# Performance work log

Hardware: AMD Instinct MI355X
Metric: run time of the kernel (lower is better)

## Reference

```python
import jax, jax.numpy as jnp
import numpy as np

DM, DI, DS, DC, DTR, L = 512, 1024, 16, 4, 32, 2
Bb, N = 4, 1024


def layer_norm(x, w, b):
    mu = x.mean(-1, keepdims=True)
    v = ((x - mu) ** 2).mean(-1, keepdims=True)
    return (x - mu) * jax.lax.rsqrt(v + 1e-5) * w + b


def silu(x):
    return x * jax.nn.sigmoid(x)


def selective_ssm(u, p):
    in_w, cw, cb, xpw, dtw, dtb, alog, dd, ow = p
    xz = u @ in_w                        # [B,N,2*DI]
    xh, z = jnp.split(xz, 2, axis=-1)
    # causal depthwise conv over time
    xt = jnp.pad(xh.transpose(0, 2, 1), ((0, 0), (0, 0), (DC - 1, 0)))
    xc = jax.lax.conv_general_dilated(xt, cw[:, None, :], (1,), 'VALID', feature_group_count=DI)
    xh = silu(xc.transpose(0, 2, 1) + cb)
    dbl = xh @ xpw                       # [B,N,DTR+2*DS]
    dt = jax.nn.softplus(dbl[..., :DTR] @ dtw + dtb)   # [B,N,DI]
    Bm = dbl[..., DTR:DTR + DS]
    Cm = dbl[..., DTR + DS:]
    A = -jnp.exp(alog)                   # [DI,DS]

    def step(h, inp):
        dt_t, B_t, C_t, x_t = inp        # [B,DI],[B,DS],[B,DS],[B,DI]
        h = jnp.exp(dt_t[..., None] * A) * h + (dt_t * x_t)[..., None] * B_t[:, None, :]
        return h, jnp.einsum('bds,bs->bd', h, C_t)

    xs = (dt.transpose(1, 0, 2), Bm.transpose(1, 0, 2), Cm.transpose(1, 0, 2), xh.transpose(1, 0, 2))
    h0 = jnp.zeros((u.shape[0], DI, DS), u.dtype)
    _, ys = jax.lax.scan(step, h0, xs)
    y = ys.transpose(1, 0, 2) + dd * xh
    return (y * silu(z)) @ ow


def mamba_layer(h, p):
    n1w, n1b, in_w, cw, cb, xpw, dtw, dtb, alog, dd, ow, n2w, n2b, w1, b1, w2, b2 = p
    h = h + selective_ssm(layer_norm(h, n1w, n1b), (in_w, cw, cb, xpw, dtw, dtb, alog, dd, ow))
    hn = layer_norm(h, n2w, n2b)
    return h + (jax.nn.gelu(hn @ w1 + b1, approximate=False) @ w2 + b2), None


def run_stack(x, stack):
    h, _ = jax.lax.scan(mamba_layer, x, stack)
    return h


def setup_inputs() -> dict:
    key = jax.random.key(0)
    ks = iter(jax.random.split(key, 80))

    def w(shape, s=0.02):
        return jax.random.normal(next(ks), shape, jnp.float32) * s

    d = {"x": jax.random.normal(next(ks), (Bb, N, DM), jnp.float32)}
    for pre in ("f", "b"):
        d[pre + "_n1w"] = jnp.ones((L, DM)); d[pre + "_n1b"] = jnp.zeros((L, DM))
        d[pre + "_inw"] = w((L, DM, 2 * DI)); d[pre + "_cw"] = w((L, DI, DC), 0.1)
        d[pre + "_cb"] = jnp.zeros((L, DI)); d[pre + "_xpw"] = w((L, DI, DTR + 2 * DS))
        d[pre + "_dtw"] = w((L, DTR, DI), 0.1); d[pre + "_dtb"] = w((L, DI), 0.5)
        d[pre + "_alog"] = jnp.tile(jnp.log(jnp.arange(1, DS + 1, dtype=jnp.float32)), (L, DI, 1))
        d[pre + "_dd"] = jnp.ones((L, DI))
        d[pre + "_ow"] = w((L, DI, DM))
        d[pre + "_n2w"] = jnp.ones((L, DM)); d[pre + "_n2b"] = jnp.zeros((L, DM))
        d[pre + "_w1"] = w((L, DM, 4 * DM)); d[pre + "_b1"] = jnp.zeros((L, 4 * DM))
        d[pre + "_w2"] = w((L, 4 * DM, DM)); d[pre + "_b2"] = jnp.zeros((L, DM))
    d["aw1"] = w((DM, DM // 2)); d["ab1"] = jnp.zeros((DM // 2,))
    d["aw2"] = w((DM // 2, 1)); d["ab2"] = jnp.zeros((1,))
    d["nw"] = jnp.ones((2 * DM,)); d["nb"] = jnp.zeros((2 * DM,))
    return d


def reference(x, f_n1w, f_n1b, f_inw, f_cw, f_cb, f_xpw, f_dtw, f_dtb, f_alog, f_dd, f_ow, f_n2w, f_n2b, f_w1, f_b1, f_w2, f_b2, b_n1w, b_n1b, b_inw, b_cw, b_cb, b_xpw, b_dtw, b_dtb, b_alog, b_dd, b_ow, b_n2w, b_n2b, b_w1, b_b1, b_w2, b_b2, aw1, ab1, aw2, ab2, nw, nb):
    fstack = (f_n1w, f_n1b, f_inw, f_cw, f_cb, f_xpw, f_dtw, f_dtb, f_alog, f_dd, f_ow, f_n2w, f_n2b, f_w1, f_b1, f_w2, f_b2)
    bstack = (b_n1w, b_n1b, b_inw, b_cw, b_cb, b_xpw, b_dtw, b_dtb, b_alog, b_dd, b_ow, b_n2w, b_n2b, b_w1, b_b1, b_w2, b_b2)
    hf = run_stack(x, fstack)
    hb = jnp.flip(run_stack(jnp.flip(x, 1), bstack), 1)

    def attn(h):
        return jax.nn.softmax((jnp.tanh(h @ aw1 + ab1) @ aw2 + ab2)[..., 0], axis=-1)

    af = attn(hf)
    abw = attn(hb)
    zf = jnp.einsum('bn,bnd->bd', af, hf)
    zb = jnp.einsum('bn,bnd->bd', abw, hb)
    z = layer_norm(jnp.concatenate([zf, zb], axis=-1), nw, nb)
    return z, (af + abw) * 0.5
```

## Files before the change

### kernel.cpp

```cpp
#include <hip/hip_runtime.h>
#include <math.h>

constexpr int kDM   = 512;
constexpr int kDI   = 1024;
constexpr int kDS   = 16;
constexpr int kDC   = 4;
constexpr int kDTR  = 32;
constexpr int kL    = 2;
constexpr int kB    = 4;
constexpr int kN    = 1024;
constexpr int kB2   = 8;
constexpr int kROWS = kB2 * kN;
constexpr int kMDIR = kB * kN;

enum { EPI_NONE=0, EPI_SOFTPLUS=1, EPI_RESID=2, EPI_GELU=3, EPI_RESID_BIAS=4, EPI_TANH=5 };
enum { MODE_N=0, MODE_OTR=1, MODE_DBL=2, MODE_GATE=3 };

typedef __attribute__((ext_vector_type(8))) short bf16x8;
typedef __attribute__((ext_vector_type(4))) short bf16x4;
typedef __attribute__((ext_vector_type(4))) float f32x4;

__device__ __forceinline__ unsigned short f2bf(float f) {
    unsigned int u = __float_as_uint(f);
    return (unsigned short)((u + 0x7FFFu + ((u >> 16) & 1u)) >> 16);
}
__device__ __forceinline__ float b2f(unsigned short u) {
    return __uint_as_float((unsigned int)u << 16);
}
__device__ __forceinline__ bf16x4 pack4(const float* v) {
    union { unsigned short u[4]; bf16x4 t; } p;
#pragma unroll
    for (int j = 0; j < 4; j++) p.u[j] = f2bf(v[j]);
    return p.t;
}

struct WJobs { const float* s[13]; };
constexpr size_t O_INW_F = 0;
constexpr size_t O_INW_B = O_INW_F + 2u*512*2048;
constexpr size_t O_XPW_F = O_INW_B + 2u*512*2048;
constexpr size_t O_XPW_B = O_XPW_F + 2u*1024*64;
constexpr size_t O_DTW_F = O_XPW_B + 2u*1024*64;
constexpr size_t O_DTW_B = O_DTW_F + 2u*32*1024;
constexpr size_t O_OW_F  = O_DTW_B + 2u*32*1024;
constexpr size_t O_OW_B  = O_OW_F  + 2u*1024*512;
constexpr size_t O_W1_F  = O_OW_B  + 2u*1024*512;
constexpr size_t O_W1_B  = O_W1_F  + 2u*512*2048;
constexpr size_t O_W2_F  = O_W1_B  + 2u*512*2048;
constexpr size_t O_W2_B  = O_W2_F  + 2u*2048*512;
constexpr size_t O_AW1   = O_W2_B  + 2u*2048*512;
constexpr size_t O_WTOT  = O_AW1   + 1u*512*256;

__global__ __launch_bounds__(256) void wprep_k(WJobs jobs, unsigned short* __restrict__ dst)
{
    const int wK[13] = {512,512,1024,1024,32,32,1024,1024,512,512,2048,2048,512};
    const int wN[13] = {2048,2048,64,64,1024,1024,512,512,2048,2048,512,512,256};
    const int wL[13] = {2,2,2,2,2,2,2,2,2,2,2,2,1};
    int blk = blockIdx.x;
    int j = 0; int base = 0; size_t doff = 0;
    for (; j < 13; j++) {
        int nb = wL[j] * (wK[j] / 32) * (wN[j] / 32);
        if (blk < base + nb) break;
        base += nb;
        doff += (size_t)wL[j] * wK[j] * wN[j];
    }
    int rel = blk - base;
    int K = wK[j], N = wN[j];
    int tk = K / 32, tn = N / 32;
    int l = rel / (tk * tn); rel -= l * tk * tn;
    int kt = rel / tn, nt = rel - (rel / tn) * tn;
    const float* src = jobs.s[j] + (size_t)l * K * N;
    unsigned short* d = dst + doff + (size_t)l * K * N;
    __shared__ float tl[32][33];
    const int c = threadIdx.x & 31, rg = threadIdx.x >> 5;
#pragma unroll
    for (int rr = 0; rr < 4; rr++)
        tl[rg * 4 + rr][c] = src[(size_t)(kt * 32 + rg * 4 + rr) * N + nt * 32 + c];
    __syncthreads();
#pragma unroll
    for (int rr = 0; rr < 4; rr++)
        d[(size_t)(nt * 32 + rg * 4 + rr) * K + kt * 32 + c] = f2bf(tl[c][rg * 4 + rr]);
}

__global__ __launch_bounds__(256) void init_h_k(const float* __restrict__ x,
                                                float* __restrict__ h)
{
    size_t idx = (size_t)blockIdx.x * 256 + threadIdx.x;
    int d  = idx & (kDM - 1);
    int t  = (idx >> 9) & (kN - 1);
    int bb = (int)(idx >> 19);
    int b = bb & 3, dir = bb >> 2;
    int ts = dir ? (kN - 1 - t) : t;
    h[idx] = x[((size_t)b * kN + ts) * kDM + d];
}

__global__ __launch_bounds__(256) void h2b_k(const float* __restrict__ h,
                                             unsigned short* __restrict__ o)
{
    size_t idx = (size_t)blockIdx.x * 256 + threadIdx.x;
    o[idx] = f2bf(h[idx]);
}

template<int DIM, int OBF>
__global__ __launch_bounds__(256) void ln_k(const float* __restrict__ x,
    const float* __restrict__ wf, const float* __restrict__ wb,
    const float* __restrict__ bf, const float* __restrict__ bbp,
    void* __restrict__ outv)
{
    const int row = blockIdx.x;
    const int tid = threadIdx.x;
    constexpr int PT = DIM / 256;
    const int dir = (row >= kMDIR) ? 1 : 0;
    const float* w = dir ? wb : wf;
    const float* b = dir ? bbp : bf;

    float v[PT];
    float s1 = 0.f, s2 = 0.f;
#pragma unroll
    for (int i = 0; i < PT; i++) {
        float t = x[(size_t)row * DIM + tid + i * 256];
        v[i] = t; s1 += t; s2 += t * t;
    }
    for (int o = 32; o > 0; o >>= 1) { s1 += __shfl_xor(s1, o, 64); s2 += __shfl_xor(s2, o, 64); }
    __shared__ float r1[4], r2[4];
    int wv = tid >> 6;
    if ((tid & 63) == 0) { r1[wv] = s1; r2[wv] = s2; }
    __syncthreads();
    s1 = r1[0] + r1[1] + r1[2] + r1[3];
    s2 = r2[0] + r2[1] + r2[2] + r2[3];
    float mu  = s1 / DIM;
    float var = s2 / DIM - mu * mu;
    float rr  = rsqrtf(var + 1e-5f);
#pragma unroll
    for (int i = 0; i < PT; i++) {
        int c = tid + i * 256;
        float o = (v[i] - mu) * rr * w[c] + b[c];
        if (OBF) ((unsigned short*)outv)[(size_t)row * DIM + c] = f2bf(o);
        else     ((float*)outv)[(size_t)row * DIM + c] = o;
    }
}

template<int BM, int BN, int EPI, int ATR, int MODE, int OBF, int KB>
__global__ __launch_bounds__(256) void gemm_mfma(
    const unsigned short* __restrict__ A, int lda, int K,
    const unsigned short* __restrict__ Btf, const unsigned short* __restrict__ Btb,
    const float* __restrict__ biasf, const float* __restrict__ biasb,
    void* __restrict__ Cv, int ldc, unsigned short* __restrict__ Ct)
{
    constexpr int SK  = 40;
    constexpr int KT  = KB / 32;
    constexpr int CPR = KB / 8;
    constexpr int WM  = BM / 2, WN = BN / 2;
    constexpr int MT  = WM / 16, NT = WN / 16;
    constexpr int ASL = (BM * KB) / (256 * 8);
    constexpr int BSL = (BN * KB) / (256 * 8);
    constexpr int MB4 = BM / 4;
    constexpr int ATR_TH = (BM / 4) * (KB / 4);
    constexpr int ATR_R  = (ATR_TH + 255) / 256;

    __shared__ unsigned short As[KT * BM * SK];
    __shared__ unsigned short Bs[KT * BN * SK];

    const int tid  = threadIdx.x;
    const int gx   = gridDim.x;
    const int nwg  = gx * gridDim.y;
    const int lin  = blockIdx.x + blockIdx.y * gx;
    const int swz  = (lin & 7) * (nwg >> 3) + (lin >> 3);
    const int by   = swz / gx;
    const int bx   = swz - by * gx;
    const int n0   = bx * BN;
    const int row0 = by * BM;
    const int dir  = (row0 >= kMDIR) ? 1 : 0;
    const unsigned short* __restrict__ Bt = dir ? Btb : Btf;
    const float* bias = dir ? biasb : biasf;

    const int lane = tid & 63;
    const int wave = tid >> 6;
    const int wr = wave >> 1, wc = wave & 1;
    const int ml = lane & 15, q = lane >> 4;

    f32x4 acc[MT][NT];
#pragma unroll
    for (int i = 0; i < MT; i++)
#pragma unroll
        for (int j = 0; j < NT; j++)
#pragma unroll
            for (int r = 0; r < 4; r++) acc[i][j][r] = 0.f;

    for (int kt = 0; kt < K; kt += KB) {
        bf16x8 a_ld[ASL ? ASL : 1];
        bf16x4 at_ld[ATR_R][4];
        if (!ATR) {
#pragma unroll
            for (int r = 0; r < ASL; r++) {
                int i = tid + r * 256;
                int m = i / CPR, c8 = (i % CPR) * 8;
                a_ld[r] = *(const bf16x8*)(A + (size_t)(row0 + m) * lda + kt + c8);
            }
        } else {
#pragma unroll
            for (int r = 0; r < ATR_R; r++) {
                int idx = tid + r * 256;
                if (idx < ATR_TH) {
                    int mb = idx % MB4, ka = idx / MB4;
#pragma unroll
                    for (int j = 0; j < 4; j++)
                        at_ld[r][j] = *(const bf16x4*)(A + (size_t)(kt + ka * 4 + j) * lda + row0 + mb * 4);
                }
            }
        }
        bf16x8 b_ld[BSL ? BSL : 1];
#pragma unroll
        for (int r = 0; r < BSL; r++) {
            int i = tid + r * 256;
            int n = i / CPR, c8 = (i % CPR) * 8;
            b_ld[r] = *(const bf16x8*)(Bt + (size_t)(n0 + n) * K + kt + c8);
        }
        __syncthreads();
        if (!ATR) {
#pragma unroll
            for (int r = 0; r < ASL; r++) {
                int i = tid + r * 256;
                int m = i / CPR, c8 = (i % CPR) * 8;
                *(bf16x8*)&As[((c8 >> 5) * BM + m) * SK + (c8 & 31)] = a_ld[r];
            }
        } else {
#pragma unroll
            for (int r = 0; r < ATR_R; r++) {
                int idx = tid + r * 256;
                if (idx < ATR_TH) {
                    int mb = idx % MB4, ka = idx / MB4;
                    union { bf16x4 v; unsigned short u[4]; } rw4[4];
#pragma unroll
                    for (int j = 0; j < 4; j++) rw4[j].v = at_ld[r][j];
                    int col = ka * 4;
#pragma unroll
                    for (int mp = 0; mp < 4; mp++) {
                        union { unsigned short u[4]; bf16x4 v; } cl;
#pragma unroll
                        for (int j = 0; j < 4; j++) cl.u[j] = rw4[j].u[mp];
                        *(bf16x4*)&As[((col >> 5) * BM + mb * 4 + mp) * SK + (col & 31)] = cl.v;
                    }
                }
            }
        }
#pragma unroll
        for (int r = 0; r < BSL; r++) {
            int i = tid + r * 256;
            int n = i / CPR, c8 = (i % CPR) * 8;
            *(bf16x8*)&Bs[((c8 >> 5) * BN + n) * SK + (c8 & 31)] = b_ld[r];
        }
        __syncthreads();
#pragma unroll
        for (int kk = 0; kk < KT; kk++) {
            bf16x8 af[MT], bfr[NT];
#pragma unroll
            for (int i = 0; i < MT; i++)
                af[i] = *(bf16x8*)&As[(kk * BM + wr * WM + i * 16 + ml) * SK + q * 8];
#pragma unroll
            for (int j = 0; j < NT; j++)
                bfr[j] = *(bf16x8*)&Bs[(kk * BN + wc * WN + j * 16 + ml) * SK + q * 8];
#pragma unroll
            for (int i = 0; i < MT; i++)
#pragma unroll
                for (int j = 0; j < NT; j++)
                    acc[i][j] = __builtin_amdgcn_mfma_f32_16x16x32_bf16(af[i], bfr[j], acc[i][j], 0, 0, 0);
        }
    }

    float* Cf = (float*)Cv;
    unsigned short* Cb = (unsigned short*)Cv;
#pragma unroll
    for (int j = 0; j < NT; j++) {
        int col = n0 + wc * WN + j * 16 + ml;
        float bv = 0.f;
        if (EPI == EPI_SOFTPLUS || EPI == EPI_GELU || EPI == EPI_RESID_BIAS || EPI == EPI_TANH)
            bv = bias[col];
#pragma unroll
        for (int i = 0; i < MT; i++) {
            int rw = row0 + wr * WM + i * 16 + q * 4;
            float v4[4];
#pragma unroll
            for (int r = 0; r < 4; r++) {
                float v = acc[i][j][r] + bv;
                if (EPI == EPI_SOFTPLUS) v = (v > 20.f) ? v : __logf(1.f + __expf(v));
                if (EPI == EPI_GELU)     v = 0.5f * v * (1.f + erff(v * 0.70710678118654752f));
                if (EPI == EPI_TANH)     v = tanhf(v);
                v4[r] = v;
            }
            if (MODE == MODE_GATE && n0 >= kDI) {
#pragma unroll
                for (int r = 0; r < 4; r++) {
                    float sv = v4[r] / (1.f + __expf(-v4[r]));
                    Ct[(size_t)(rw + r) * kDI + (col - kDI)] = f2bf(sv);
                }
            } else {
#pragma unroll
                for (int r = 0; r < 4; r++) {
                    size_t o = (size_t)(rw + r) * ldc + col;
                    if (EPI == EPI_RESID || EPI == EPI_RESID_BIAS) Cf[o] += v4[r];
                    else if (OBF) Cb[o] = f2bf(v4[r]);
                    else Cf[o] = v4[r];
                }
                if (MODE == MODE_DBL && col >= 32) {
                    float* F = (float*)Ct;
#pragma unroll
                    for (int r = 0; r < 4; r++)
                        F[(size_t)(rw + r) * 32 + (col - 32)] = v4[r];
                }
            }
        }
    }
}

__global__ __launch_bounds__(256) void conv_k(const unsigned short* __restrict__ xb,
    const float* __restrict__ cwf, const float* __restrict__ cwb,
    const float* __restrict__ cbf, const float* __restrict__ cbb,
    unsigned short* __restrict__ xh)
{
    __shared__ float tl[67][33];
    const int t0 = blockIdx.x * 64, d0 = blockIdx.y * 32, bb = blockIdx.z;
    const int dir = bb >> 2;
    const float* cw = dir ? cwb : cwf;
    const float* cb = dir ? cbb : cbf;
    const int dl = threadIdx.x & 31, rl = threadIdx.x >> 5;
    const size_t base = (size_t)bb * kN * kDI + d0 + dl;
#pragma unroll
    for (int p = 0; p < 9; p++) {
        int r = p * 8 + rl;
        if (r < 67) {
            int ts = t0 + r - 3;
            tl[r][dl] = (ts >= 0) ? b2f(xb[base + (size_t)ts * kDI]) : 0.f;
        }
    }
    __syncthreads();
    const int gd = d0 + dl;
    float c0 = cw[gd*4+0], c1 = cw[gd*4+1], c2 = cw[gd*4+2], c3 = cw[gd*4+3];
    float bv = cb[gd];
#pragma unroll
    for (int jj = 0; jj < 8; jj++) {
        int tt = rl + 8 * jj;
        float acc = bv + c0*tl[tt][dl] + c1*tl[tt+1][dl] + c2*tl[tt+2][dl] + c3*tl[tt+3][dl];
        float o = acc / (1.f + __expf(-acc));
        xh[(size_t)(bb * kN + t0 + tt) * kDI + gd] = f2bf(o);
    }
}

constexpr int kG  = 32;
constexpr int kTg = kN / kG;

template<int PASS>
__global__ __launch_bounds__(256) void bscan_k(
    const unsigned short* __restrict__ dt,
    const unsigned short* __restrict__ xh,
    const unsigned short* __restrict__ gate,
    const float* __restrict__ dblF,
    unsigned short* __restrict__ y,
    float* __restrict__ PL,
    const float* __restrict__ alogf, const float* __restrict__ alogb,
    const float* __restrict__ ddf,   const float* __restrict__ ddb)
{
    const int d  = blockIdx.x * 256 + threadIdx.x;
    const int g  = blockIdx.y;
    const int bb = blockIdx.z;
    const int dir = bb >> 2;
    const float* alog = dir ? alogb : alogf;
    const float* ddp  = dir ? ddb  : ddf;

    float a2[16];
#pragma unroll
    for (int s = 0; s < 16; s += 4) {
        float4 al = *(const float4*)&alog[d * kDS + s];
        a2[s+0] = -__expf(al.x) * 1.44269504f;
        a2[s+1] = -__expf(al.y) * 1.44269504f;
        a2[s+2] = -__expf(al.z) * 1.44269504f;
        a2[s+3] = -__expf(al.w) * 1.44269504f;
    }

    const size_t plb = (size_t)(bb * kG + g) * 32 * kDI + d;
    float h[16];
    if (PASS == 0) {
#pragma unroll
        for (int s = 0; s < 16; s++) h[s] = 0.f;
    } else {
#pragma unroll
        for (int s = 0; s < 16; s++) h[s] = PL[plb + (size_t)(16 + s) * kDI];
    }

    const int row0 = bb * kN + g * kTg;
    const unsigned short* pd = dt   + (size_t)row0 * kDI + d;
    const unsigned short* px = xh   + (size_t)row0 * kDI + d;
    const unsigned short* pg = gate + (size_t)row0 * kDI + d;
    const float* pbc = dblF + (size_t)row0 * 32;
    unsigned short* py = y + (size_t)row0 * kDI + d;
    const float ddv = ddp[d];
    float sdt = 0.f;

#pragma unroll 4
    for (int t = 0; t < kTg; t++) {
        float dtv = b2f(pd[(size_t)t * kDI]);
        float xvv = b2f(px[(size_t)t * kDI]);
        float dtx = dtv * xvv;
        const float* bc = pbc + t * 32;
        if (PASS == 0) {
            sdt += dtv;
#pragma unroll
            for (int s4 = 0; s4 < 4; s4++) {
                float4 Bq = *(const float4*)(bc + s4 * 4);
                h[s4*4+0] = __builtin_amdgcn_exp2f(dtv * a2[s4*4+0]) * h[s4*4+0] + dtx * Bq.x;
                h[s4*4+1] = __builtin_amdgcn_exp2f(dtv * a2[s4*4+1]) * h[s4*4+1] + dtx * Bq.y;
                h[s4*4+2] = __builtin_amdgcn_exp2f(dtv * a2[s4*4+2]) * h[s4*4+2] + dtx * Bq.z;
                h[s4*4+3] = __builtin_amdgcn_exp2f(dtv * a2[s4*4+3]) * h[s4*4+3] + dtx * Bq.w;
            }
        } else {
            float p = 0.f;
#pragma unroll
            for (int s4 = 0; s4 < 4; s4++) {
                float4 Bq = *(const float4*)(bc + s4 * 4);
                float4 Cq = *(const float4*)(bc + 16 + s4 * 4);
                h[s4*4+0] = __builtin_amdgcn_exp2f(dtv * a2[s4*4+0]) * h[s4*4+0] + dtx * Bq.x;
                p += h[s4*4+0] * Cq.x;
                h[s4*4+1] = __builtin_amdgcn_exp2f(dtv * a2[s4*4+1]) * h[s4*4+1] + dtx * Bq.y;
                p += h[s4*4+1] * Cq.y;
                h[s4*4+2] = __builtin_amdgcn_exp2f(dtv * a2[s4*4+2]) * h[s4*4+2] + dtx * Bq.z;
                p += h[s4*4+2] * Cq.z;
                h[s4*4+3] = __builtin_amdgcn_exp2f(dtv * a2[s4*4+3]) * h[s4*4+3] + dtx * Bq.w;
                p += h[s4*4+3] * Cq.w;
            }
            float gvv = b2f(pg[(size_t)t * kDI]);
            py[(size_t)t * kDI] = f2bf((p + ddv * xvv) * gvv);
        }
    }

    if (PASS == 0) {
#pragma unroll
        for (int s = 0; s < 16; s++) {
            PL[plb + (size_t)s * kDI]        = __builtin_amdgcn_exp2f(a2[s] * sdt);
            PL[plb + (size_t)(16 + s) * kDI] = h[s];
        }
    }
}

__global__ __launch_bounds__(256) void bfix_k(float* __restrict__ PL)
{
    const int idx = blockIdx.x * 256 + threadIdx.x;
    const int d  = idx & (kDI - 1);
    const int bb = (idx >> 10) & 7;
    const int s  = idx >> 13;
    float h = 0.f;
    for (int g = 0; g < kG; g++) {
        size_t base = (size_t)(bb * kG + g) * 32 * kDI + d;
        float P = PL[base + (size_t)s * kDI];
        float L = PL[base + (size_t)(16 + s) * kDI];
        PL[base + (size_t)(16 + s) * kDI] = h;
        h = P * h + L;
    }
}

__global__ __launch_bounds__(64) void att_score_k(const unsigned short* __restrict__ tmp,
    const float* __restrict__ aw2, const float* __restrict__ ab2,
    float* __restrict__ score)
{
    int row = blockIdx.x, lane = threadIdx.x;
    float acc = 0.f;
#pragma unroll
    for (int j = 0; j < 4; j++)
        acc += b2f(tmp[(size_t)row * 256 + lane + j * 64]) * aw2[lane + j * 64];
    for (int o = 32; o > 0; o >>= 1) acc += __shfl_xor(acc, o, 64);
    if (lane == 0) score[row] = acc + ab2[0];
}

__global__ __launch_bounds__(256) void softmax_k(const float* __restrict__ score,
                                                 float* __restrict__ w)
{
    int bb = blockIdx.x, tid = threadIdx.x;
    float v[4]; float m = -1e30f;
#pragma unroll
    for (int i = 0; i < 4; i++) { v[i] = score[bb * kN + tid + i * 256]; m = fmaxf(m, v[i]); }
    for (int o = 32; o > 0; o >>= 1) m = fmaxf(m, __shfl_xor(m, o, 64));
    __shared__ float r1[4], r2[4];
    int wv = tid >> 6;
    if ((tid & 63) == 0) r1[wv] = m;
    __syncthreads();
    m = fmaxf(fmaxf(r1[0], r1[1]), fmaxf(r1[2], r1[3]));
    float s = 0.f;
#pragma unroll
    for (int i = 0; i < 4; i++) { v[i] = __expf(v[i] - m); s += v[i]; }
    for (int o = 32; o > 0; o >>= 1) s += __shfl_xor(s, o, 64);
    if ((tid & 63) == 0) r2[wv] = s;
    __syncthreads();
    s = r2[0] + r2[1] + r2[2] + r2[3];
    float inv = 1.f / s;
#pragma unroll
    for (int i = 0; i < 4; i++) w[bb * kN + tid + i * 256] = v[i] * inv;
}

__global__ __launch_bounds__(512) void pool_k(const float* __restrict__ w,
    const float* __restrict__ h, float* zcat)
{
    int bb = blockIdx.x, chunk = blockIdx.y;
    int d = threadIdx.x;
    float acc = 0.f;
    int n0 = chunk * 32;
    for (int n = n0; n < n0 + 32; n++)
        acc += w[bb * kN + n] * h[((size_t)bb * kN + n) * kDM + d];
    int b = bb & 3, dir = bb >> 2;
    atomicAdd(&zcat[b * (2 * kDM) + dir * kDM + d], acc);
}

__global__ __launch_bounds__(256) void att_out_k(const float* __restrict__ w,
                                                 float* __restrict__ out)
{
    int idx = blockIdx.x * 256 + threadIdx.x;
    int b = idx >> 10, n = idx & 1023;
    out[idx] = 0.5f * (w[b * kN + n] + w[(b + 4) * kN + (kN - 1 - n)]);
}

extern "C" void kernel_launch(void* const* d_in, const int* in_sizes, int n_in,
                              void* d_out, int out_size, void* d_ws, size_t ws_size,
                              hipStream_t stream)
{
    const float* x = (const float*)d_in[0];
    const float* fp[17]; const float* bp[17];
    for (int i = 0; i < 17; i++) { fp[i] = (const float*)d_in[1 + i]; bp[i] = (const float*)d_in[18 + i]; }
    const float* aw1 = (const float*)d_in[35];
    const float* ab1 = (const float*)d_in[36];
    const float* aw2 = (const float*)d_in[37];
    const float* ab2 = (const float*)d_in[38];
    const float* nw  = (const float*)d_in[39];
    const float* nb  = (const float*)d_in[40];
    float* out = (float*)d_out;

    float* h = (float*)d_ws;
    unsigned short* ub    = (unsigned short*)(h + (size_t)kROWS * kDM);
    unsigned short* xbuf  = ub    + (size_t)kROWS * kDM;
    unsigned short* tbuf  = xbuf  + (size_t)kROWS * kDI;
    unsigned short* xhb   = tbuf  + (size_t)kROWS * kDI;
    unsigned short* gateb = xhb   + (size_t)kROWS * kDI;
    unsigned short* dbl   = gateb + (size_t)kROWS * kDI;
    float* dblF  = (float*)(dbl + (size_t)kROWS * 64);
    float* score = dblF + (size_t)kROWS * 32;
    float* smw   = score + kROWS;
    float* zcat  = smw   + kROWS;
    unsigned short* wts  = (unsigned short*)(zcat + kB * 2 * kDM);
    float* PL = (float*)(wts + O_WTOT);

    WJobs jobs;
    jobs.s[0] = fp[2];  jobs.s[1] = bp[2];
    jobs.s[2] = fp[5];  jobs.s[3] = bp[5];
    jobs.s[4] = fp[6];  jobs.s[5] = bp[6];
    jobs.s[6] = fp[10]; jobs.s[7] = bp[10];
    jobs.s[8] = fp[13]; jobs.s[9] = bp[13];
    jobs.s[10] = fp[15]; jobs.s[11] = bp[15];
    jobs.s[12] = aw1;
    int wblocks = 0;
    {
        const int wK[13] = {512,512,1024,1024,32,32,1024,1024,512,512,2048,2048,512};
        const int wN[13] = {2048,2048,64,64,1024,1024,512,512,2048,2048,512,512,256};
        const int wL[13] = {2,2,2,2,2,2,2,2,2,2,2,2,1};
        for (int j = 0; j < 13; j++) wblocks += wL[j] * (wK[j]/32) * (wN[j]/32);
    }
    wprep_k<<<wblocks, 256, 0, stream>>>(jobs, wts);

    init_h_k<<<kROWS * kDM / 256, 256, 0, stream>>>(x, h);

    for (int l = 0; l < kL; l++) {
        const float *f_n1w = fp[0]  + l * kDM,            *b_n1w = bp[0]  + l * kDM;
        const float *f_n1b = fp[1]  + l * kDM,            *b_n1b = bp[1]  + l * kDM;
        const float *f_cw  = fp[3]  + l * kDI * kDC,      *b_cw  = bp[3]  + l * kDI * kDC;
        const float *f_cb  = fp[4]  + l * kDI,            *b_cb  = bp[4]  + l * kDI;
        const float *f_dtb = fp[7]  + l * kDI,            *b_dtb = bp[7]  + l * kDI;
        const float *f_alog= fp[8]  + l * kDI * kDS,      *b_alog= bp[8]  + l * kDI * kDS;
        const float *f_dd  = fp[9]  + l * kDI,            *b_dd  = bp[9]  + l * kDI;
        const float *f_n2w = fp[11] + l * kDM,            *b_n2w = bp[11] + l * kDM;
        const float *f_n2b = fp[12] + l * kDM,            *b_n2b = bp[12] + l * kDM;
        const float *f_b1  = fp[14] + l * 4 * kDM,        *b_b1  = bp[14] + l * 4 * kDM;
        const float *f_b2  = fp[16] + l * kDM,            *b_b2  = bp[16] + l * kDM;

        const unsigned short *wInwF = wts + O_INW_F + (size_t)l * 2048 * 512;
        const unsigned short *wInwB = wts + O_INW_B + (size_t)l * 2048 * 512;
        const unsigned short *wXpwF = wts + O_XPW_F + (size_t)l * 64 * 1024;
        const unsigned short *wXpwB = wts + O_XPW_B + (size_t)l * 64 * 1024;
        const unsigned short *wDtwF = wts + O_DTW_F + (size_t)l * 1024 * 32;
        const unsigned short *wDtwB = wts + O_DTW_B + (size_t)l * 1024 * 32;
        const unsigned short *wOwF  = wts + O_OW_F  + (size_t)l * 512 * 1024;
        const unsigned short *wOwB  = wts + O_OW_B  + (size_t)l * 512 * 1024;
        const unsigned short *wW1F  = wts + O_W1_F  + (size_t)l * 2048 * 512;
        const unsigned short *wW1B  = wts + O_W1_B  + (size_t)l * 2048 * 512;
        const unsigned short *wW2F  = wts + O_W2_F  + (size_t)l * 512 * 2048;
        const unsigned short *wW2B  = wts + O_W2_B  + (size_t)l * 512 * 2048;

        ln_k<kDM,1><<<kROWS, 256, 0, stream>>>(h, f_n1w, b_n1w, f_n1b, b_n1b, ub);
        gemm_mfma<128,128,EPI_NONE,0,MODE_GATE,1,64><<<dim3(16, 64), 256, 0, stream>>>(
            ub, kDM, kDM, wInwF, wInwB, nullptr, nullptr, xbuf, kDI, gateb);
        conv_k<<<dim3(kN/64, kDI/32, kB2), 256, 0, stream>>>(
            xbuf, f_cw, b_cw, f_cb, b_cb, xhb);
        gemm_mfma<32,64,EPI_NONE,0,MODE_DBL,1,64><<<dim3(1, 256), 256, 0, stream>>>(
            xhb, kDI, kDI, wXpwF, wXpwB, nullptr, nullptr, dbl, 64, (unsigned short*)dblF);
        gemm_mfma<128,128,EPI_SOFTPLUS,0,MODE_N,1,32><<<dim3(8, 64), 256, 0, stream>>>(
            dbl, 64, kDTR, wDtwF, wDtwB, f_dtb, b_dtb, tbuf, kDI, nullptr);
        bscan_k<0><<<dim3(kDI/256, kG, kB2), 256, 0, stream>>>(
            tbuf, xhb, gateb, dblF, xbuf, PL, f_alog, b_alog, f_dd, b_dd);
        bfix_k<<<kB2 * kDI * kDS / 256, 256, 0, stream>>>(PL);
        bscan_k<1><<<dim3(kDI/256, kG, kB2), 256, 0, stream>>>(
            tbuf, xhb, gateb, dblF, xbuf, PL, f_alog, b_alog, f_dd, b_dd);
        gemm_mfma<128,64,EPI_RESID,0,MODE_N,0,64><<<dim3(8, 64), 256, 0, stream>>>(
            xbuf, kDI, kDI, wOwF, wOwB, nullptr, nullptr, h, kDM, nullptr);
        ln_k<kDM,1><<<kROWS, 256, 0, stream>>>(h, f_n2w, b_n2w, f_n2b, b_n2b, ub);
        gemm_mfma<128,128,EPI_GELU,0,MODE_N,1,64><<<dim3(16, 64), 256, 0, stream>>>(
            ub, kDM, kDM, wW1F, wW1B, f_b1, b_b1, xbuf, 4*kDM, nullptr);
        gemm_mfma<128,64,EPI_RESID_BIAS,0,MODE_N,0,64><<<dim3(8, 64), 256, 0, stream>>>(
            xbuf, 4*kDM, 4*kDM, wW2F, wW2B, f_b2, b_b2, h, kDM, nullptr);
    }

    h2b_k<<<kROWS * kDM / 256, 256, 0, stream>>>(h, tbuf);
    gemm_mfma<64,128,EPI_TANH,0,MODE_N,1,64><<<dim3(2, 128), 256, 0, stream>>>(
        tbuf, kDM, kDM, wts + O_AW1, wts + O_AW1, ab1, ab1, ub, 256, nullptr);
    att_score_k<<<kROWS, 64, 0, stream>>>(ub, aw2, ab2, score);
    softmax_k<<<kB2, 256, 0, stream>>>(score, smw);
    hipMemsetAsync(zcat, 0, kB * 2 * kDM * sizeof(float), stream);
    pool_k<<<dim3(kB2, 32), 512, 0, stream>>>(smw, h, zcat);
    ln_k<2*kDM,0><<<kB, 256, 0, stream>>>(zcat, nw, nw, nb, nb, out);
    att_out_k<<<kB * kN / 256, 256, 0, stream>>>(smw, out + kB * 2 * kDM);
}
```

Measured before the change: 727.8 us.

## Load GEMM tiles directly global-to-LDS with XOR-swizzled layout for KB=64

For KB=64 GEMM instantiations, tiles are now loaded with global_load_lds 16-byte direct transfers into a compact XOR-swizzled LDS layout instead of going through registers into padded shared memory. The fragment reads apply the matching XOR to avoid bank conflicts. This removes the register staging and the VGPR pressure of the copy. The transposed-A (ATR) load path is dropped, and the fallback path gains an extra barrier at the end of each iteration. The change relies on the per-lane LDS address layout of global_load_lds being correct, and any ATR users would now read A untransposed.

```diff
diff --git a/kernel.cpp b/kernel.cpp
--- a/kernel.cpp
+++ b/kernel.cpp
@@ -27,12 +27,10 @@
 __device__ __forceinline__ float b2f(unsigned short u) {
     return __uint_as_float((unsigned int)u << 16);
 }
-__device__ __forceinline__ bf16x4 pack4(const float* v) {
-    union { unsigned short u[4]; bf16x4 t; } p;
-#pragma unroll
-    for (int j = 0; j < 4; j++) p.u[j] = f2bf(v[j]);
-    return p.t;
-}
+
+#define GLD_LDS16(gsrc, ldst) \
+    __builtin_amdgcn_global_load_lds((const __attribute__((address_space(1))) void*)(gsrc), \
+                                     (__attribute__((address_space(3))) void*)(ldst), 16, 0, 0)
 
 struct WJobs { const float* s[13]; };
 constexpr size_t O_INW_F = 0;
@@ -153,12 +151,11 @@
     constexpr int MT  = WM / 16, NT = WN / 16;
     constexpr int ASL = (BM * KB) / (256 * 8);
     constexpr int BSL = (BN * KB) / (256 * 8);
-    constexpr int MB4 = BM / 4;
-    constexpr int ATR_TH = (BM / 4) * (KB / 4);
-    constexpr int ATR_R  = (ATR_TH + 255) / 256;
-
-    __shared__ unsigned short As[KT * BM * SK];
-    __shared__ unsigned short Bs[KT * BN * SK];
+    constexpr int ASZ = (KB == 64) ? BM * 64 : KT * BM * SK;
+    constexpr int BSZ = (KB == 64) ? BN * 64 : KT * BN * SK;
+
+    __shared__ __align__(16) unsigned short As[ASZ];
+    __shared__ __align__(16) unsigned short Bs[BSZ];
 
     const int tid  = threadIdx.x;
     const int gx   = gridDim.x;
@@ -186,84 +183,100 @@
 #pragma unroll
             for (int r = 0; r < 4; r++) acc[i][j][r] = 0.f;
 
-    for (int kt = 0; kt < K; kt += KB) {
-        bf16x8 a_ld[ASL ? ASL : 1];
-        bf16x4 at_ld[ATR_R][4];
-        if (!ATR) {
+    if constexpr (KB == 64) {
+        constexpr int ACW = BM / 32;
+        constexpr int BCW = BN / 32;
+        const int lrow = lane >> 3;
+        const int lcol = ((lane & 7) ^ (lrow & 7)) << 4;
+        const char* aS[ACW ? ACW : 1];
+        const char* bS[BCW ? BCW : 1];
+#pragma unroll
+        for (int ch = 0; ch < ACW; ch++) {
+            const int chunk = wave * ACW + ch;
+            aS[ch] = (const char*)A + (size_t)(row0 + chunk * 8 + lrow) * lda * 2 + lcol;
+        }
+#pragma unroll
+        for (int ch = 0; ch < BCW; ch++) {
+            const int chunk = wave * BCW + ch;
+            bS[ch] = (const char*)Bt + (size_t)(n0 + chunk * 8 + lrow) * K * 2 + lcol;
+        }
+        const int axor = (ml & 7) << 3;
+
+        for (int kt = 0; kt < K; kt += 64) {
+#pragma unroll
+            for (int ch = 0; ch < ACW; ch++) {
+                GLD_LDS16(aS[ch], &As[(wave * ACW + ch) * 512]);
+                aS[ch] += 128;
+            }
+#pragma unroll
+            for (int ch = 0; ch < BCW; ch++) {
+                GLD_LDS16(bS[ch], &Bs[(wave * BCW + ch) * 512]);
+                bS[ch] += 128;
+            }
+            __syncthreads();
+#pragma unroll
+            for (int kk = 0; kk < 2; kk++) {
+                bf16x8 af[MT], bfr[NT];
+#pragma unroll
+                for (int i = 0; i < MT; i++)
+                    af[i] = *(bf16x8*)&As[(wr * WM + i * 16 + ml) * 64 + ((kk * 32 + q * 8) ^ axor)];
+#pragma unroll
+                for (int j = 0; j < NT; j++)
+                    bfr[j] = *(bf16x8*)&Bs[(wc * WN + j * 16 + ml) * 64 + ((kk * 32 + q * 8) ^ axor)];
+#pragma unroll
+                for (int i = 0; i < MT; i++)
+#pragma unroll
+                    for (int j = 0; j < NT; j++)
+                        acc[i][j] = __builtin_amdgcn_mfma_f32_16x16x32_bf16(af[i], bfr[j], acc[i][j], 0, 0, 0);
+            }
+            __syncthreads();
+        }
+    } else {
+        for (int kt = 0; kt < K; kt += KB) {
+            bf16x8 a_ld[ASL ? ASL : 1];
 #pragma unroll
             for (int r = 0; r < ASL; r++) {
                 int i = tid + r * 256;
                 int m = i / CPR, c8 = (i % CPR) * 8;
                 a_ld[r] = *(const bf16x8*)(A + (size_t)(row0 + m) * lda + kt + c8);
             }
-        } else {
-#pragma unroll
-            for (int r = 0; r < ATR_R; r++) {
-                int idx = tid + r * 256;
-                if (idx < ATR_TH) {
-                    int mb = idx % MB4, ka = idx / MB4;
-#pragma unroll
-                    for (int j = 0; j < 4; j++)
-                        at_ld[r][j] = *(const bf16x4*)(A + (size_t)(kt + ka * 4 + j) * lda + row0 + mb * 4);
-                }
-            }
-        }
-        bf16x8 b_ld[BSL ? BSL : 1];
-#pragma unroll
-        for (int r = 0; r < BSL; r++) {
-            int i = tid + r * 256;
-            int n = i / CPR, c8 = (i % CPR) * 8;
-            b_ld[r] = *(const bf16x8*)(Bt + (size_t)(n0 + n) * K + kt + c8);
-        }
-        __syncthreads();
-        if (!ATR) {
+            bf16x8 b_ld[BSL ? BSL : 1];
+#pragma unroll
+            for (int r = 0; r < BSL; r++) {
+                int i = tid + r * 256;
+                int n = i / CPR, c8 = (i % CPR) * 8;
+                b_ld[r] = *(const bf16x8*)(Bt + (size_t)(n0 + n) * K + kt + c8);
+            }
+            __syncthreads();
 #pragma unroll
             for (int r = 0; r < ASL; r++) {
                 int i = tid + r * 256;
                 int m = i / CPR, c8 = (i % CPR) * 8;
                 *(bf16x8*)&As[((c8 >> 5) * BM + m) * SK + (c8 & 31)] = a_ld[r];
             }
-        } else {
-#pragma unroll
-            for (int r = 0; r < ATR_R; r++) {
-                int idx = tid + r * 256;
-                if (idx < ATR_TH) {
-                    int mb = idx % MB4, ka = idx / MB4;
-                    union { bf16x4 v; unsigned short u[4]; } rw4[4];
-#pragma unroll
-                    for (int j = 0; j < 4; j++) rw4[j].v = at_ld[r][j];
-                    int col = ka * 4;
-#pragma unroll
-                    for (int mp = 0; mp < 4; mp++) {
-                        union { unsigned short u[4]; bf16x4 v; } cl;
-#pragma unroll
-                        for (int j = 0; j < 4; j++) cl.u[j] = rw4[j].u[mp];
-                        *(bf16x4*)&As[((col >> 5) * BM + mb * 4 + mp) * SK + (col & 31)] = cl.v;
-                    }
-                }
-            }
-        }
-#pragma unroll
-        for (int r = 0; r < BSL; r++) {
-            int i = tid + r * 256;
-            int n = i / CPR, c8 = (i % CPR) * 8;
-            *(bf16x8*)&Bs[((c8 >> 5) * BN + n) * SK + (c8 & 31)] = b_ld[r];
-        }
-        __syncthreads();
-#pragma unroll
-        for (int kk = 0; kk < KT; kk++) {
-            bf16x8 af[MT], bfr[NT];
-#pragma unroll
-            for (int i = 0; i < MT; i++)
-                af[i] = *(bf16x8*)&As[(kk * BM + wr * WM + i * 16 + ml) * SK + q * 8];
-#pragma unroll
-            for (int j = 0; j < NT; j++)
-                bfr[j] = *(bf16x8*)&Bs[(kk * BN + wc * WN + j * 16 + ml) * SK + q * 8];
-#pragma unroll
-            for (int i = 0; i < MT; i++)
+#pragma unroll
+            for (int r = 0; r < BSL; r++) {
+                int i = tid + r * 256;
+                int n = i / CPR, c8 = (i % CPR) * 8;
+                *(bf16x8*)&Bs[((c8 >> 5) * BN + n) * SK + (c8 & 31)] = b_ld[r];
+            }
+            __syncthreads();
+#pragma unroll
+            for (int kk = 0; kk < KT; kk++) {
+                bf16x8 af[MT], bfr[NT];
+#pragma unroll
+                for (int i = 0; i < MT; i++)
+                    af[i] = *(bf16x8*)&As[(kk * BM + wr * WM + i * 16 + ml) * SK + q * 8];
 #pragma unroll
                 for (int j = 0; j < NT; j++)
-                    acc[i][j] = __builtin_amdgcn_mfma_f32_16x16x32_bf16(af[i], bfr[j], acc[i][j], 0, 0, 0);
+                    bfr[j] = *(bf16x8*)&Bs[(kk * BN + wc * WN + j * 16 + ml) * SK + q * 8];
+#pragma unroll
+                for (int i = 0; i < MT; i++)
+#pragma unroll
+                    for (int j = 0; j < NT; j++)
+                        acc[i][j] = __builtin_amdgcn_mfma_f32_16x16x32_bf16(af[i], bfr[j], acc[i][j], 0, 0, 0);
+            }
+            __syncthreads();
         }
     }
 
```

New measurement: 711.6 us. -2.2%, faster.
